# Performance work log

Hardware: AMD Instinct MI355X
Metric: run time of the kernel (lower is better)

## Reference

```python
import jax, jax.numpy as jnp
import numpy as np

BS, SD, SL, HS = 8, 200, 96, 64
GDEP = 2
ALPHA = 0.1
EPS = 1e-5


def _ln(x, g, b):
    # LayerNorm over the last 3 dims (matches nn.LayerNorm([d1,d2,d3]))
    mu = x.mean((-3, -2, -1), keepdims=True)
    var = x.var((-3, -2, -1), keepdims=True)
    return (x - mu) * jax.lax.rsqrt(var + EPS) * g + b


def _gru(x, Wih, Whh, bih, bhh):
    # single-layer batch_first GRU, returns output sequence. x: [B, L, H]
    B, L, H = x.shape
    xw = x @ Wih.T + bih  # precompute input projections [B, L, 3H]

    def step(h, xw_t):
        gh = h @ Whh.T + bhh
        xr, xz, xn = jnp.split(xw_t, 3, -1)
        hr, hz, hn = jnp.split(gh, 3, -1)
        r = jax.nn.sigmoid(xr + hr)
        z = jax.nn.sigmoid(xz + hz)
        n = jnp.tanh(xn + r * hn)
        h = (1.0 - z) * n + z * h
        return h, h

    _, ys = jax.lax.scan(step, jnp.zeros((B, H), x.dtype), jnp.swapaxes(xw, 0, 1))
    return jnp.swapaxes(ys, 0, 1)


def _norm_adj(A):
    # add self loops, row-normalize (MTGNN mixprop preprocessing)
    Ah = A + jnp.eye(A.shape[-1], dtype=A.dtype)
    return Ah / Ah.sum(-1, keepdims=True)


def _mixprop(x, a, W, b):
    # x: [B, C, V, L], a: [V, V] (static graph)
    h = x
    outs = [h]
    for _ in range(GDEP):
        h = ALPHA * x + (1.0 - ALPHA) * jnp.einsum('bcwl,vw->bcvl', h, a)
        outs.append(h)
    ho = jnp.concatenate(outs, axis=1)  # [B, (GDEP+1)C, V, L]
    return jnp.einsum('bcvl,oc->bovl', ho, W) + b[None, :, None, None]


def _dyna_mixprop(x, a, W, b):
    # x: [B, C, V, L], a: [B, L, V, W] (per-batch, per-time dynamic graph)
    h = x
    outs = [h]
    for _ in range(GDEP):
        h = ALPHA * x + (1.0 - ALPHA) * jnp.einsum('bcwl,blvw->bcvl', h, a)
        outs.append(h)
    ho = jnp.concatenate(outs, axis=1)
    return jnp.einsum('bcvl,oc->bovl', ho, W) + b[None, :, None, None]


def _fwd(x, adj, dyna_adj, g1, b1, g2, b2, Wih, Whh, bih, bhh,
         Wg1, bg1, Wg2, bg2, Wd1, bd1, Wd2, bd2, Wm, bm):
    bs, sd, sl, hs = x.shape
    # RNN encoder over time with residual
    xr = _gru(_ln(x, g1, b1).reshape(bs * sd, sl, hs), Wih, Whh, bih, bhh) \
        + x.reshape(bs * sd, sl, hs)
    xc = xr.reshape(bs, sd, sl, hs).transpose(0, 3, 1, 2)  # [bs, hs, sd, sl]
    nx = _ln(xc, g2, b2)
    a = _norm_adj(adj)
    at = _norm_adj(adj.T)
    da = _norm_adj(dyna_adj)
    dat = _norm_adj(jnp.swapaxes(dyna_adj, -1, -2))
    x_static = (_mixprop(nx, a, Wg1, bg1) + _mixprop(nx, at, Wg2, bg2)).transpose(0, 2, 3, 1)
    x_dyna = (_dyna_mixprop(nx, da, Wd1, bd1) + _dyna_mixprop(nx, dat, Wd2, bd2)).transpose(0, 2, 3, 1)
    merged = jnp.concatenate([x_static, x_dyna], axis=-1) @ Wm.T + bm
    return merged + xc.transpose(0, 2, 3, 1)  # [bs, sd, sl, hs]


def setup_inputs() -> dict:
    key = jax.random.key(0)
    ks = jax.random.split(key, 20)
    s = 0.02
    C3 = (GDEP + 1) * HS
    return {
        'x': jax.random.normal(ks[0], (BS, SD, SL, HS), jnp.float32),
        'adj': jax.random.uniform(ks[1], (SD, SD), jnp.float32),
        'dyna_adj': jax.random.uniform(ks[2], (BS, SL, SD, SD), jnp.float32),
        'g1': 1.0 + s * jax.random.normal(ks[3], (SD, SL, HS), jnp.float32),
        'b1': s * jax.random.normal(ks[4], (SD, SL, HS), jnp.float32),
        'g2': 1.0 + s * jax.random.normal(ks[5], (HS, SD, SL), jnp.float32),
        'b2': s * jax.random.normal(ks[6], (HS, SD, SL), jnp.float32),
        'Wih': s * jax.random.normal(ks[7], (3 * HS, HS), jnp.float32),
        'Whh': s * jax.random.normal(ks[8], (3 * HS, HS), jnp.float32),
        'bih': jnp.zeros((3 * HS,), jnp.float32),
        'bhh': jnp.zeros((3 * HS,), jnp.float32),
        'Wg1': s * jax.random.normal(ks[9], (HS, C3), jnp.float32),
        'bg1': jnp.zeros((HS,), jnp.float32),
        'Wg2': s * jax.random.normal(ks[10], (HS, C3), jnp.float32),
        'bg2': jnp.zeros((HS,), jnp.float32),
        'Wd1': s * jax.random.normal(ks[11], (HS, C3), jnp.float32),
        'bd1': jnp.zeros((HS,), jnp.float32),
        'Wd2': s * jax.random.normal(ks[12], (HS, C3), jnp.float32),
        'bd2': jnp.zeros((HS,), jnp.float32),
        'Wm': s * jax.random.normal(ks[13], (HS, 2 * HS), jnp.float32),
        'bm': jnp.zeros((HS,), jnp.float32),
    }


def reference(x, adj, dyna_adj, g1, b1, g2, b2, Wih, Whh, bih, bhh,
              Wg1, bg1, Wg2, bg2, Wd1, bd1, Wd2, bd2, Wm, bm):
    return _fwd(x, adj, dyna_adj, g1, b1, g2, b2, Wih, Whh, bih, bhh,
                Wg1, bg1, Wg2, bg2, Wd1, bd1, Wd2, bd2, Wm, bm)
```

## Files before the change

### kernel.cpp

```cpp
#include <hip/hip_runtime.h>
#include <math.h>

#define ALPHA_ 0.1f
#define BETA_  0.9f
#define EPS_   1e-5f

typedef __bf16 bf16x8 __attribute__((ext_vector_type(8)));
typedef float f32x16 __attribute__((ext_vector_type(16)));

__device__ __forceinline__ unsigned short f2bf(float f) {
    return __builtin_bit_cast(unsigned short, (__bf16)f);
}
__device__ __forceinline__ float bf2f(unsigned short u) {
    return (float)__builtin_bit_cast(__bf16, u);
}

__device__ __forceinline__ float wave_reduce_sum(float v) {
#pragma unroll
    for (int off = 32; off > 0; off >>= 1) v += __shfl_down(v, off, 64);
    return v;
}

__global__ void k_ln_part(const float4* __restrict__ x4, float2* __restrict__ part) {
    const int b = blockIdx.y, jb = blockIdx.x, t = threadIdx.x;
    const size_t base = (size_t)b * 307200 + (size_t)jb * 4096;
    float s = 0.f, sq = 0.f;
#pragma unroll
    for (int k = 0; k < 16; k++) {
        float4 v = x4[base + k * 256 + t];
        s  += v.x + v.y + v.z + v.w;
        sq += v.x * v.x + v.y * v.y + v.z * v.z + v.w * v.w;
    }
    float rs = wave_reduce_sum(s);
    float rq = wave_reduce_sum(sq);
    __shared__ float2 ws[4];
    if ((t & 63) == 0) ws[t >> 6] = make_float2(rs, rq);
    __syncthreads();
    if (t == 0) {
        float a = 0.f, q = 0.f;
        for (int k = 0; k < 4; k++) { a += ws[k].x; q += ws[k].y; }
        part[b * 75 + jb] = make_float2(a, q);
    }
}

__global__ void k_ln_final(const float2* __restrict__ part, int nper, float2* __restrict__ outp) {
    const int b = blockIdx.x, t = threadIdx.x;
    float s = 0.f, sq = 0.f;
    for (int p = t; p < nper; p += 64) {
        float2 v = part[b * nper + p];
        s += v.x; sq += v.y;
    }
    s  = wave_reduce_sum(s);
    sq = wave_reduce_sum(sq);
    if (t == 0) {
        const float invN = 1.f / 1228800.f;
        float mu  = s * invN;
        float var = sq * invN - mu * mu;
        outp[b] = make_float2(mu, rsqrtf(var + EPS_));
    }
}

__global__ __launch_bounds__(256) void k_xw2(const float* __restrict__ x,
        const float* __restrict__ g1, const float* __restrict__ b1,
        const float2* __restrict__ s1, const float* __restrict__ Wih,
        const float* __restrict__ bih, unsigned short* __restrict__ xw) {
    __shared__ unsigned short sXb[128 * 64];
    __shared__ unsigned short sWb[192 * 64];
    const int t = threadIdx.x;
    const int R0 = blockIdx.x * 128;
    const float2 st1 = s1[R0 / 19200];
    for (int idx = t; idx < 8192; idx += 256) {
        int rr = idx >> 6, cc = idx & 63;
        int row = R0 + rr;
        int gi = (row % 19200) * 64 + cc;
        float v = (x[(size_t)row * 64 + cc] - st1.x) * st1.y * g1[gi] + b1[gi];
        *(unsigned short*)((char*)sXb + ((rr * 128 + cc * 2) ^ ((rr & 7) << 4))) = f2bf(v);
    }
    for (int idx = t; idx < 12288; idx += 256) {
        int j = idx >> 6, k = idx & 63;
        *(unsigned short*)((char*)sWb + ((j * 128 + k * 2) ^ ((j & 7) << 4))) = f2bf(Wih[idx]);
    }
    __syncthreads();
    const int wid = t >> 6, lane = t & 63, ln = lane & 31, hl = lane >> 5;
    f32x16 acc[6] = {};
#pragma unroll
    for (int ks = 0; ks < 4; ks++) {
        int ao = ((wid * 32 + ln) * 128 + ks * 32 + hl * 16) ^ ((ln & 7) << 4);
        bf16x8 af = __builtin_bit_cast(bf16x8, *(const uint4*)((const char*)sXb + ao));
#pragma unroll
        for (int nt = 0; nt < 6; nt++) {
            int bo = ((nt * 32 + ln) * 128 + ks * 32 + hl * 16) ^ ((ln & 7) << 4);
            bf16x8 bfr = __builtin_bit_cast(bf16x8, *(const uint4*)((const char*)sWb + bo));
            acc[nt] = __builtin_amdgcn_mfma_f32_32x32x16_bf16(af, bfr, acc[nt], 0, 0, 0);
        }
    }
#pragma unroll
    for (int nt = 0; nt < 6; nt++) {
        float bi = bih[nt * 32 + ln];
#pragma unroll
        for (int reg = 0; reg < 16; reg++) {
            int rrow = (reg & 3) + 8 * (reg >> 2) + 4 * hl;
            int row = R0 + wid * 32 + rrow;
            xw[(size_t)row * 192 + nt * 32 + ln] = f2bf(acc[nt][reg] + bi);
        }
    }
}

__global__ __launch_bounds__(512) void k_gru2(const unsigned short* __restrict__ xw,
        const float* __restrict__ x, const float* __restrict__ Whh,
        const float* __restrict__ bhh, float* __restrict__ xr, float2* __restrict__ s2p) {
    __shared__ unsigned short hb[2048];
    __shared__ float gh[1536];
    __shared__ float2 sRed[8];
    const int t = threadIdx.x;
    const int wid = t >> 6, lane = t & 63, ln = lane & 31, hl = lane >> 5;
    const int row0 = blockIdx.x * 8;
    const int r = wid;
    const int c = t & 63;

    bf16x8 Bf[4];
    if (wid < 6) {
        const int j = wid * 32 + ln;
#pragma unroll
        for (int ks = 0; ks < 4; ks++) {
            const float* wp = Whh + j * 64 + ks * 16 + hl * 8;
            float4 w0 = *(const float4*)wp;
            float4 w1 = *(const float4*)(wp + 4);
            bf16x8 bb;
            bb[0] = (__bf16)w0.x; bb[1] = (__bf16)w0.y; bb[2] = (__bf16)w0.z; bb[3] = (__bf16)w0.w;
            bb[4] = (__bf16)w1.x; bb[5] = (__bf16)w1.y; bb[6] = (__bf16)w1.z; bb[7] = (__bf16)w1.w;
            Bf[ks] = bb;
        }
    }
    for (int i = t; i < 2048; i += 512) hb[i] = 0;

    const float b_r = bhh[c], b_z = bhh[64 + c], b_n = bhh[128 + c];
    const unsigned short* xwp = xw + (size_t)(row0 + r) * 96 * 192;
    const float* xp  = x  + (size_t)(row0 + r) * 96 * 64;
    float*       xrp = xr + (size_t)(row0 + r) * 96 * 64;
    float xg = bf2f(xwp[c]), zg = bf2f(xwp[64 + c]), ng = bf2f(xwp[128 + c]);
    float xv = xp[c];
    float h = 0.f, lsum = 0.f, lsq = 0.f;
    __syncthreads();

    for (int st = 0; st < 96; st++) {
        if (wid < 6) {
            f32x16 acc = {};
#pragma unroll
            for (int ks = 0; ks < 4; ks++) {
                int ao = (ln * 128 + ks * 32 + hl * 16) ^ ((ln & 7) << 4);
                bf16x8 af = __builtin_bit_cast(bf16x8, *(const uint4*)((const char*)hb + ao));
                acc = __builtin_amdgcn_mfma_f32_32x32x16_bf16(af, Bf[ks], acc, 0, 0, 0);
            }
#pragma unroll
            for (int reg = 0; reg < 4; reg++) {
                gh[(reg + 4 * hl) * 192 + wid * 32 + ln] = acc[reg];
            }
        }
        __syncthreads();
        float hr_ = gh[r * 192 + c] + b_r;
        float hz  = gh[r * 192 + 64 + c] + b_z;
        float hn  = gh[r * 192 + 128 + c] + b_n;
        float rg_ = 1.f / (1.f + __expf(-(xg + hr_)));
        float zg_ = 1.f / (1.f + __expf(-(zg + hz)));
        float ny = ng + rg_ * hn;
        ny = fminf(fmaxf(ny, -15.f), 15.f);
        float e2 = __expf(-2.f * ny);
        float nv = (1.f - e2) / (1.f + e2);
        h = nv + zg_ * (h - nv);
        float ov = h + xv;
        xrp[st * 64 + c] = ov;
        lsum += ov; lsq += ov * ov;
        *(unsigned short*)((char*)hb + ((r * 128 + c * 2) ^ ((r & 7) << 4))) = f2bf(h);
        int sn = st < 95 ? st + 1 : 95;
        xg = bf2f(xwp[sn * 192 + c]); zg = bf2f(xwp[sn * 192 + 64 + c]); ng = bf2f(xwp[sn * 192 + 128 + c]);
        xv = xp[sn * 64 + c];
        __syncthreads();
    }
    float s = wave_reduce_sum(lsum);
    float q = wave_reduce_sum(lsq);
    if (lane == 0) sRed[wid] = make_float2(s, q);
    __syncthreads();
    if (t == 0) {
        float a = 0.f, b_ = 0.f;
        for (int k = 0; k < 8; k++) { a += sRed[k].x; b_ += sRed[k].y; }
        s2p[blockIdx.x] = make_float2(a, b_);
    }
}

__global__ void k_tr(const float* __restrict__ in, float* __restrict__ outp) {
    __shared__ float tile[32][33];
    const int v = blockIdx.x;
    const int ct = blockIdx.y & 1;
    const int lt = blockIdx.y >> 1;
    const int t = threadIdx.x;
    const int lx = t & 31, ly = t >> 5;
    const int c0 = ct * 32, l0 = lt * 32;
#pragma unroll
    for (int q = 0; q < 4; q++) {
        int cc = ly + q * 8;
        tile[cc][lx] = in[(size_t)(c0 + cc) * 19200 + (size_t)v * 96 + l0 + lx];
    }
    __syncthreads();
#pragma unroll
    for (int q = 0; q < 4; q++) {
        int ll = ly + q * 8;
        outp[(size_t)(l0 + ll) * 12800 + (size_t)v * 64 + c0 + lx] = tile[lx][ll];
    }
}

__global__ void k_adjprep2(const float* __restrict__ adj, unsigned short* __restrict__ an_b,
        unsigned short* __restrict__ atn_b) {
    const int v = blockIdx.x;
    const int mode = blockIdx.y;
    const int t = threadIdx.x;
    unsigned short* outp = (mode == 0) ? an_b : atn_b;
    float val = 0.f;
    if (t < 200) val = (mode == 0) ? adj[v * 200 + t] : adj[t * 200 + v];
    float s = wave_reduce_sum(val);
    __shared__ float sp[4];
    if ((t & 63) == 0) sp[t >> 6] = s;
    __syncthreads();
    float inv = 1.f / (sp[0] + sp[1] + sp[2] + sp[3] + 1.f);
    if (t < 208) {
        float o = (t < 200) ? (val + (t == v ? 1.f : 0.f)) * inv : 0.f;
        outp[(((t >> 3) * 200) + v) * 8 + (t & 7)] = f2bf(o);
    }
}

__global__ __launch_bounds__(512) void k_dprep4(const float* __restrict__ dyna,
        unsigned short* __restrict__ danr, unsigned short* __restrict__ danc) {
    __shared__ unsigned short sT[200 * 201];
    __shared__ float sRow[200];
    __shared__ float sColP[8][256];
    __shared__ float sInv[416];
    const int blk = blockIdx.x;
    const int t = threadIdx.x;
    const int lane = t & 63, rq = t >> 6;
    const float* S = dyna + (size_t)blk * 40000;
    float colacc[4] = {0.f, 0.f, 0.f, 0.f};
    for (int p = 0; p < 25; p++) {
        const int r = p * 8 + rq;
        float rsum = 0.f;
#pragma unroll
        for (int s = 0; s < 4; s++) {
            const int c = s * 64 + lane;
            if (c < 200) {
                float v = S[r * 200 + c] + ((r == c) ? 1.f : 0.f);
                sT[c * 201 + r] = f2bf(v);
                rsum += v;
                colacc[s] += v;
            }
        }
        float rs = wave_reduce_sum(rsum);
        if (lane == 0) sRow[r] = rs;
    }
#pragma unroll
    for (int s = 0; s < 4; s++) sColP[rq][s * 64 + lane] = colacc[s];
    __syncthreads();
    if (t < 200) {
        sInv[t] = 1.f / sRow[t];
        float cs = 0.f;
#pragma unroll
        for (int q = 0; q < 8; q++) cs += sColP[q][t];
        sInv[208 + t] = 1.f / cs;
    }
    __syncthreads();
    unsigned short* dr = danr + (size_t)blk * 41600;
    unsigned short* dc = danc + (size_t)blk * 41600;
    for (int item = t; item < 5200; item += 512) {
        const int cch = item / 200;
        const int v = item - cch * 200;
        const float irv = sInv[v];
        const float icv = sInv[208 + v];
        unsigned short rb[8], cb[8];
#pragma unroll
        for (int j = 0; j < 8; j++) {
            const int w = cch * 8 + j;
            float fr = 0.f, fc = 0.f;
            if (w < 200) {
                fr = bf2f(sT[w * 201 + v]) * irv;
                fc = bf2f(sT[v * 201 + w]) * icv;
            }
            rb[j] = f2bf(fr); cb[j] = f2bf(fc);
        }
        *(uint4*)&dr[item * 8] = make_uint4(
            (unsigned)rb[0] | ((unsigned)rb[1] << 16), (unsigned)rb[2] | ((unsigned)rb[3] << 16),
            (unsigned)rb[4] | ((unsigned)rb[5] << 16), (unsigned)rb[6] | ((unsigned)rb[7] << 16));
        *(uint4*)&dc[item * 8] = make_uint4(
            (unsigned)cb[0] | ((unsigned)cb[1] << 16), (unsigned)cb[2] | ((unsigned)cb[3] << 16),
            (unsigned)cb[4] | ((unsigned)cb[5] << 16), (unsigned)cb[6] | ((unsigned)cb[7] << 16));
    }
}

__global__ void k_meff(const float* __restrict__ Wm, const float* __restrict__ Wg1,
        const float* __restrict__ Wg2, const float* __restrict__ Wd1, const float* __restrict__ Wd2,
        const float* __restrict__ bg1, const float* __restrict__ bg2, const float* __restrict__ bd1,
        const float* __restrict__ bd2, const float* __restrict__ bm,
        float* __restrict__ MeffF, float* __restrict__ biasE) {
    const int k = blockIdx.x;
    const int t = threadIdx.x;
    const int o = t >> 2;
    const int cb = (t & 3) * 16;
    float acc[16];
#pragma unroll
    for (int q = 0; q < 16; q++) acc[q] = 0.f;
    if (k == 0) {
        for (int m = 0; m < 64; m++) {
            float aL = Wm[o * 128 + m], aR = Wm[o * 128 + 64 + m];
#pragma unroll
            for (int q = 0; q < 16; q++) {
                int cc = cb + q;
                acc[q] += aL * (Wg1[m * 192 + cc] + Wg2[m * 192 + cc])
                        + aR * (Wd1[m * 192 + cc] + Wd2[m * 192 + cc]);
            }
        }
    } else {
        const float* Ws = (k <= 2) ? Wg1 : (k <= 4) ? Wg2 : (k <= 6) ? Wd1 : Wd2;
        const int side = (k <= 4) ? 0 : 64;
        const int hop = (((k - 1) & 1) == 0) ? 64 : 128;
        for (int m = 0; m < 64; m++) {
            float a_ = Wm[o * 128 + side + m];
#pragma unroll
            for (int q = 0; q < 16; q++) acc[q] += a_ * Ws[m * 192 + hop + cb + q];
        }
    }
#pragma unroll
    for (int q = 0; q < 16; q++) MeffF[k * 4096 + o * 64 + cb + q] = acc[q];
    if (k == 0 && t < 64) {
        float s = bm[t];
        for (int cc = 0; cc < 64; cc++)
            s += Wm[t * 128 + cc] * (bg1[cc] + bg2[cc]) + Wm[t * 128 + 64 + cc] * (bd1[cc] + bd2[cc]);
        biasE[t] = s;
    }
}

__global__ void k_meffc(const float* __restrict__ MeffF, unsigned short* __restrict__ MeffB) {
    const int t = threadIdx.x;
#pragma unroll 4
    for (int j = 0; j < 16; j++) {
        int idx = t * 16 + j;
        float m[9];
#pragma unroll
        for (int k = 0; k < 9; k++) m[k] = MeffF[k * 4096 + idx];
        float sum = 0.f;
#pragma unroll
        for (int k = 1; k < 9; k++) sum += m[k];
        MeffB[idx] = f2bf(m[0] + ALPHA_ * sum);
#pragma unroll
        for (int c = 0; c < 4; c++) {
            MeffB[(1 + 2 * c) * 4096 + idx] = f2bf(BETA_ * m[1 + 2 * c] + ALPHA_ * BETA_ * m[2 + 2 * c]);
            MeffB[(2 + 2 * c) * 4096 + idx] = f2bf(BETA_ * BETA_ * m[2 + 2 * c]);
        }
    }
}

__global__ void k_nx(const float4* __restrict__ xr4, const float2* __restrict__ s2,
        const float4* __restrict__ g2t4, const float4* __restrict__ b2t4,
        unsigned short* __restrict__ nxb) {
    size_t id = (size_t)blockIdx.x * 256 + threadIdx.x;
    int cf = (int)(id & 15);
    size_t grp = id >> 4;
    int v = (int)(grp % 200);
    size_t bl = grp / 200;
    int l = (int)(bl % 96);
    int b = (int)(bl / 96);
    float2 st = s2[b];
    float4 xv = xr4[(((size_t)(b * 200 + v)) * 96 + l) * 16 + cf];
    size_t gi = ((size_t)l * 200 + v) * 16 + cf;
    float4 g = g2t4[gi];
    float4 bb = b2t4[gi];
    unsigned int lo = (unsigned)f2bf((xv.x - st.x) * st.y * g.x + bb.x)
                    | ((unsigned)f2bf((xv.y - st.x) * st.y * g.y + bb.y) << 16);
    unsigned int hi = (unsigned)f2bf((xv.z - st.x) * st.y * g.z + bb.z)
                    | ((unsigned)f2bf((xv.w - st.x) * st.y * g.w + bb.w) << 16);
    ((uint2*)nxb)[id] = make_uint2(lo, hi);
}

#define OFF_A 0
#define OFF_HTA 83968
#define OFF_HTB 110592
#define OFF_OBUF 0
#define SMEM10 137216

__device__ __forceinline__ int ht4(int o, int w) {
    return (o * 416 + w * 2) ^ ((o & 7) << 4);
}

__device__ __forceinline__ void store_tile_bf16(unsigned char* smem, int off, const f32x16& val,
        int mt, int ocol, int half) {
#pragma unroll
    for (int g = 0; g < 4; g++) {
        const int wv = mt * 32 + half * 4 + g * 8;
        if (wv < 200) {
            unsigned short pk[4];
#pragma unroll
            for (int i = 0; i < 4; i++) pk[i] = f2bf(val[g * 4 + i]);
            *(uint2*)(smem + off + ht4(ocol, wv)) = make_uint2(
                (unsigned)pk[0] | ((unsigned)pk[1] << 16),
                (unsigned)pk[2] | ((unsigned)pk[3] << 16));
        }
    }
}

__device__ __forceinline__ void stageA(const unsigned short* __restrict__ A,
        unsigned char* smem, int t) {
#pragma unroll
    for (int i = 0; i < 5; i++) {
        const int idx = t + i * 1024;
        __builtin_amdgcn_global_load_lds(
            (const __attribute__((address_space(1))) unsigned int*)(const void*)(A + (size_t)idx * 8),
            (__attribute__((address_space(3))) unsigned int*)(void*)(smem + OFF_A + idx * 16),
            16, 0, 0);
    }
    if (t < 80) {
        const int idx = 5120 + t;
        *(uint4*)(smem + OFF_A + idx * 16) = *(const uint4*)(const void*)(A + (size_t)idx * 8);
    }
}

__global__ __launch_bounds__(1024) void k_graph10(const unsigned short* __restrict__ nxb,
        const float* __restrict__ xrb, const unsigned short* __restrict__ an_b,
        const unsigned short* __restrict__ atn_b, const unsigned short* __restrict__ danr_b,
        const unsigned short* __restrict__ danc_b, const unsigned short* __restrict__ MeffB,
        const float* __restrict__ biasE, float* __restrict__ out) {
    __shared__ __align__(16) unsigned char smem[SMEM10];
    const int blk = blockIdx.x;
    const int b = blk / 96, l = blk % 96;
    const int t = threadIdx.x;
    const int wid = t >> 6, lane = t & 63, ln = lane & 31, half = lane >> 5;
    const bool act = (wid < 14);
    const int mt = wid >> 1, ot = wid & 1;
    const int ocol = ot * 32 + ln;
    const int vr = mt * 32 + ln;
    const int ar = (vr < 200) ? vr : 0;
    const bool vz = (vr >= 200);

    const unsigned short* Achain[4] = { an_b, atn_b,
        danr_b + (size_t)blk * 41600, danc_b + (size_t)blk * 41600 };

    uint4 h0f[4] = {};
    if (act && !vz) {
        const unsigned short* H0p = nxb + (size_t)blk * 12800 + vr * 64;
#pragma unroll
        for (int kk = 0; kk < 4; kk++) {
            h0f[kk] = *(const uint4*)(const void*)(H0p + kk * 16 + half * 8);
        }
    }

    stageA(Achain[0], smem, t);
    if (t < 512) {
        int o = t >> 3, w = 200 + (t & 7);
        *(unsigned short*)(smem + OFF_HTA + ht4(o, w)) = 0;
        *(unsigned short*)(smem + OFF_HTB + ht4(o, w)) = 0;
    }
    __syncthreads();

    f32x16 ACC = {};
    if (act) {
        const unsigned short* MBf = MeffB;
        const unsigned short* MB2 = MeffB + 2 * 4096;
        f32x16 y2 = {};
#pragma unroll
        for (int kk = 0; kk < 4; kk++) {
            const int c0 = kk * 16 + half * 8;
            bf16x8 h0 = __builtin_bit_cast(bf16x8, h0f[kk]);
            bf16x8 mf = __builtin_bit_cast(bf16x8, *(const uint4*)(const void*)(MBf + ocol * 64 + c0));
            ACC = __builtin_amdgcn_mfma_f32_32x32x16_bf16(h0, mf, ACC, 0, 0, 0);
            bf16x8 m2 = __builtin_bit_cast(bf16x8, *(const uint4*)(const void*)(MB2 + ocol * 64 + c0));
            y2 = __builtin_amdgcn_mfma_f32_32x32x16_bf16(h0, m2, y2, 0, 0, 0);
        }
        store_tile_bf16(smem, OFF_HTA, y2, mt, ocol, half);
    }
    __syncthreads();

#pragma unroll 1
    for (int chain = 0; chain < 4; chain++) {
        if (act) {
            const unsigned short* MB1 = MeffB + (size_t)(1 + 2 * chain) * 4096;
            f32x16 T = {};
#pragma unroll
            for (int kk = 0; kk < 4; kk++) {
                const int c0 = kk * 16 + half * 8;
                bf16x8 h0 = __builtin_bit_cast(bf16x8, h0f[kk]);
                bf16x8 m1 = __builtin_bit_cast(bf16x8, *(const uint4*)(const void*)(MB1 + ocol * 64 + c0));
                T = __builtin_amdgcn_mfma_f32_32x32x16_bf16(h0, m1, T, 0, 0, 0);
            }
#pragma unroll
            for (int kk = 0; kk < 13; kk++) {
                const int k0 = kk * 16 + half * 8;
                uint4 av = *(const uint4*)(smem + OFF_A + (((2 * kk + half) * 200 + ar) << 4));
                if (vz) av = make_uint4(0, 0, 0, 0);
                bf16x8 yb = __builtin_bit_cast(bf16x8, *(const uint4*)(smem + OFF_HTA + ht4(ocol, k0)));
                T = __builtin_amdgcn_mfma_f32_32x32x16_bf16(
                    __builtin_bit_cast(bf16x8, av), yb, T, 0, 0, 0);
            }
            store_tile_bf16(smem, OFF_HTB, T, mt, ocol, half);
        }
        __syncthreads();
        if (act) {
#pragma unroll
            for (int kk = 0; kk < 13; kk++) {
                const int k0 = kk * 16 + half * 8;
                uint4 av = *(const uint4*)(smem + OFF_A + (((2 * kk + half) * 200 + ar) << 4));
                if (vz) av = make_uint4(0, 0, 0, 0);
                bf16x8 ub = __builtin_bit_cast(bf16x8, *(const uint4*)(smem + OFF_HTB + ht4(ocol, k0)));
                ACC = __builtin_amdgcn_mfma_f32_32x32x16_bf16(
                    __builtin_bit_cast(bf16x8, av), ub, ACC, 0, 0, 0);
            }
        }
        __syncthreads();
        if (chain < 3) {
            stageA(Achain[chain + 1], smem, t);
            if (act) {
                const unsigned short* MB2n = MeffB + (size_t)(4 + 2 * chain) * 4096;
                f32x16 y2 = {};
#pragma unroll
                for (int kk = 0; kk < 4; kk++) {
                    const int c0 = kk * 16 + half * 8;
                    bf16x8 h0 = __builtin_bit_cast(bf16x8, h0f[kk]);
                    bf16x8 m2 = __builtin_bit_cast(bf16x8, *(const uint4*)(const void*)(MB2n + ocol * 64 + c0));
                    y2 = __builtin_amdgcn_mfma_f32_32x32x16_bf16(h0, m2, y2, 0, 0, 0);
                }
                store_tile_bf16(smem, OFF_HTA, y2, mt, ocol, half);
            }
            __syncthreads();
        }
    }

    __syncthreads();
    if (act) {
#pragma unroll
        for (int r = 0; r < 16; r++) {
            const int v = mt * 32 + half * 4 + (r & 3) + (r >> 2) * 8;
            if (v < 200) *(float*)(smem + OFF_OBUF + (v * 64 + ocol) * 4) = ACC[r];
        }
    }
    __syncthreads();

    const size_t gbase = ((size_t)b * 200 * 96 + l) * 64;
    for (int idx = t; idx < 12800; idx += 1024) {
        int v = idx >> 6, o = idx & 63;
        float val = *(const float*)(smem + OFF_OBUF + idx * 4) + biasE[o];
        size_t gi = gbase + (size_t)v * 6144 + o;
        out[gi] = val + xrb[gi];
    }
}

extern "C" void kernel_launch(void* const* d_in, const int* in_sizes, int n_in,
                              void* d_out, int out_size, void* d_ws, size_t ws_size,
                              hipStream_t stream) {
    (void)in_sizes; (void)n_in; (void)out_size; (void)ws_size;
    const float* x    = (const float*)d_in[0];
    const float* adj  = (const float*)d_in[1];
    const float* dyna = (const float*)d_in[2];
    const float* g1   = (const float*)d_in[3];
    const float* b1   = (const float*)d_in[4];
    const float* g2   = (const float*)d_in[5];
    const float* b2   = (const float*)d_in[6];
    const float* Wih  = (const float*)d_in[7];
    const float* Whh  = (const float*)d_in[8];
    const float* bih  = (const float*)d_in[9];
    const float* bhh  = (const float*)d_in[10];
    const float* Wg1  = (const float*)d_in[11];
    const float* bg1  = (const float*)d_in[12];
    const float* Wg2  = (const float*)d_in[13];
    const float* bg2  = (const float*)d_in[14];
    const float* Wd1  = (const float*)d_in[15];
    const float* bd1  = (const float*)d_in[16];
    const float* Wd2  = (const float*)d_in[17];
    const float* bd2  = (const float*)d_in[18];
    const float* Wm   = (const float*)d_in[19];
    const float* bm   = (const float*)d_in[20];
    float* out = (float*)d_out;
    float* ws = (float*)d_ws;

    float*          xr    = ws;
    unsigned short* nxb   = (unsigned short*)(ws + 9830400);
    float*          g2t   = ws + 14745600;
    float*          b2t   = ws + 15974400;
    unsigned short* an_b  = (unsigned short*)(ws + 17203200);
    unsigned short* atn_b = (unsigned short*)(ws + 17226496);
    unsigned short* MeffB = (unsigned short*)(ws + 17249792);
    float*          biasE = ws + 17268224;
    float2*         s1p   = (float2*)(ws + 17268288);
    float2*         s1    = (float2*)(ws + 17269488);
    float2*         s2p   = (float2*)(ws + 17269504);
    float2*         s2    = (float2*)(ws + 17269904);
    float*          MeffF = ws + 17269920;
    unsigned short* xwb    = (unsigned short*)(ws + 17306784);
    unsigned short* danr_b = (unsigned short*)(ws + 17306784);
    unsigned short* danc_b = danr_b + 31953792;

    k_ln_part<<<dim3(75, 8), dim3(256), 0, stream>>>((const float4*)x, s1p);
    k_ln_final<<<dim3(8), dim3(64), 0, stream>>>(s1p, 75, s1);
    k_xw2<<<dim3(1200), dim3(256), 0, stream>>>(x, g1, b1, s1, Wih, bih, xwb);
    k_gru2<<<dim3(200), dim3(512), 0, stream>>>(xwb, x, Whh, bhh, xr, s2p);
    k_ln_final<<<dim3(8), dim3(64), 0, stream>>>(s2p, 25, s2);
    k_tr<<<dim3(200, 6), dim3(256), 0, stream>>>(g2, g2t);
    k_tr<<<dim3(200, 6), dim3(256), 0, stream>>>(b2, b2t);
    k_adjprep2<<<dim3(200, 2), dim3(256), 0, stream>>>(adj, an_b, atn_b);
    k_meff<<<dim3(9), dim3(256), 0, stream>>>(Wm, Wg1, Wg2, Wd1, Wd2, bg1, bg2, bd1, bd2, bm, MeffF, biasE);
    k_meffc<<<dim3(1), dim3(256), 0, stream>>>(MeffF, MeffB);
    k_nx<<<dim3(9600), dim3(256), 0, stream>>>((const float4*)xr, s2, (const float4*)g2t, (const float4*)b2t, nxb);
    k_dprep4<<<dim3(768), dim3(512), 0, stream>>>(dyna, danr_b, danc_b);
    k_graph10<<<dim3(768), dim3(1024), 0, stream>>>(nxb, xr, an_b, atn_b, danr_b, danc_b, MeffB, biasE, out);
}
```

Before: 436.5 us.

## Fuse GRU input projection into recurrent kernel and widen dyna-adj prep blocks

Drops the separate input-projection GEMM kernel. The recurrent GRU kernel now applies the first LayerNorm on the fly and computes x·Wih together with h·Whh in one MFMA chain of K=128, with separate n-gate accumulators so r·hn stays correct. This removes the bf16 xw intermediate write and read, but puts extra MFMA work and global loads of x/g1/b1 on the serial 96-step critical path. The dynamic-adjacency prep kernel also moves from 512 to 1024 threads per block to spread the row loop across more waves.

```diff
diff --git a/kernel.cpp b/kernel.cpp
--- a/kernel.cpp
+++ b/kernel.cpp
@@ -60,70 +60,33 @@
     }
 }
 
-__global__ __launch_bounds__(256) void k_xw2(const float* __restrict__ x,
+__global__ __launch_bounds__(512) void k_gru3(const float* __restrict__ x,
         const float* __restrict__ g1, const float* __restrict__ b1,
         const float2* __restrict__ s1, const float* __restrict__ Wih,
-        const float* __restrict__ bih, unsigned short* __restrict__ xw) {
-    __shared__ unsigned short sXb[128 * 64];
-    __shared__ unsigned short sWb[192 * 64];
-    const int t = threadIdx.x;
-    const int R0 = blockIdx.x * 128;
-    const float2 st1 = s1[R0 / 19200];
-    for (int idx = t; idx < 8192; idx += 256) {
-        int rr = idx >> 6, cc = idx & 63;
-        int row = R0 + rr;
-        int gi = (row % 19200) * 64 + cc;
-        float v = (x[(size_t)row * 64 + cc] - st1.x) * st1.y * g1[gi] + b1[gi];
-        *(unsigned short*)((char*)sXb + ((rr * 128 + cc * 2) ^ ((rr & 7) << 4))) = f2bf(v);
-    }
-    for (int idx = t; idx < 12288; idx += 256) {
-        int j = idx >> 6, k = idx & 63;
-        *(unsigned short*)((char*)sWb + ((j * 128 + k * 2) ^ ((j & 7) << 4))) = f2bf(Wih[idx]);
-    }
-    __syncthreads();
-    const int wid = t >> 6, lane = t & 63, ln = lane & 31, hl = lane >> 5;
-    f32x16 acc[6] = {};
-#pragma unroll
-    for (int ks = 0; ks < 4; ks++) {
-        int ao = ((wid * 32 + ln) * 128 + ks * 32 + hl * 16) ^ ((ln & 7) << 4);
-        bf16x8 af = __builtin_bit_cast(bf16x8, *(const uint4*)((const char*)sXb + ao));
-#pragma unroll
-        for (int nt = 0; nt < 6; nt++) {
-            int bo = ((nt * 32 + ln) * 128 + ks * 32 + hl * 16) ^ ((ln & 7) << 4);
-            bf16x8 bfr = __builtin_bit_cast(bf16x8, *(const uint4*)((const char*)sWb + bo));
-            acc[nt] = __builtin_amdgcn_mfma_f32_32x32x16_bf16(af, bfr, acc[nt], 0, 0, 0);
-        }
-    }
-#pragma unroll
-    for (int nt = 0; nt < 6; nt++) {
-        float bi = bih[nt * 32 + ln];
-#pragma unroll
-        for (int reg = 0; reg < 16; reg++) {
-            int rrow = (reg & 3) + 8 * (reg >> 2) + 4 * hl;
-            int row = R0 + wid * 32 + rrow;
-            xw[(size_t)row * 192 + nt * 32 + ln] = f2bf(acc[nt][reg] + bi);
-        }
-    }
-}
-
-__global__ __launch_bounds__(512) void k_gru2(const unsigned short* __restrict__ xw,
-        const float* __restrict__ x, const float* __restrict__ Whh,
+        const float* __restrict__ Whh, const float* __restrict__ bih,
         const float* __restrict__ bhh, float* __restrict__ xr, float2* __restrict__ s2p) {
-    __shared__ unsigned short hb[2048];
-    __shared__ float gh[1536];
+    __shared__ unsigned short hb[32 * 128];
+    __shared__ float gh[8 * 192];
+    __shared__ float ghn[8 * 64];
     __shared__ float2 sRed[8];
     const int t = threadIdx.x;
     const int wid = t >> 6, lane = t & 63, ln = lane & 31, hl = lane >> 5;
     const int row0 = blockIdx.x * 8;
     const int r = wid;
     const int c = t & 63;
-
-    bf16x8 Bf[4];
+    const int row = row0 + r;
+    const int sd = row % 200;
+    const int bidx = row / 200;
+    const bool isN = (wid >= 4 && wid < 6);
+
+    bf16x8 Bf[8];
     if (wid < 6) {
         const int j = wid * 32 + ln;
 #pragma unroll
-        for (int ks = 0; ks < 4; ks++) {
-            const float* wp = Whh + j * 64 + ks * 16 + hl * 8;
+        for (int ks = 0; ks < 8; ks++) {
+            const float* Wsrc = (ks < 4) ? Wih : Whh;
+            const int kk = (ks & 3) * 16 + hl * 8;
+            const float* wp = Wsrc + j * 64 + kk;
             float4 w0 = *(const float4*)wp;
             float4 w1 = *(const float4*)(wp + 4);
             bf16x8 bb;
@@ -132,38 +95,66 @@
             Bf[ks] = bb;
         }
     }
-    for (int i = t; i < 2048; i += 512) hb[i] = 0;
-
-    const float b_r = bhh[c], b_z = bhh[64 + c], b_n = bhh[128 + c];
-    const unsigned short* xwp = xw + (size_t)(row0 + r) * 96 * 192;
-    const float* xp  = x  + (size_t)(row0 + r) * 96 * 64;
-    float*       xrp = xr + (size_t)(row0 + r) * 96 * 64;
-    float xg = bf2f(xwp[c]), zg = bf2f(xwp[64 + c]), ng = bf2f(xwp[128 + c]);
+    for (int i = t; i < 4096; i += 512) hb[i] = 0;
+    __syncthreads();
+
+    const float b_r = bih[c] + bhh[c];
+    const float b_z = bih[64 + c] + bhh[64 + c];
+    const float bx_n = bih[128 + c];
+    const float bh_n = bhh[128 + c];
+    const float2 st1 = s1[bidx];
+    const float* xp  = x  + (size_t)row * 96 * 64;
+    const float* gp  = g1 + (size_t)sd * 96 * 64;
+    const float* bp  = b1 + (size_t)sd * 96 * 64;
+    float*       xrp = xr + (size_t)row * 96 * 64;
+
     float xv = xp[c];
+    {
+        float xln = (xv - st1.x) * st1.y * gp[c] + bp[c];
+        *(unsigned short*)((char*)hb + ((r * 256 + c * 2) ^ ((r & 7) << 4))) = f2bf(xln);
+    }
     float h = 0.f, lsum = 0.f, lsq = 0.f;
     __syncthreads();
 
     for (int st = 0; st < 96; st++) {
-        if (wid < 6) {
+        if (wid < 4) {
             f32x16 acc = {};
 #pragma unroll
-            for (int ks = 0; ks < 4; ks++) {
-                int ao = (ln * 128 + ks * 32 + hl * 16) ^ ((ln & 7) << 4);
+            for (int ks = 0; ks < 8; ks++) {
+                int ao = (ln * 256 + ks * 32 + hl * 16) ^ ((ln & 7) << 4);
                 bf16x8 af = __builtin_bit_cast(bf16x8, *(const uint4*)((const char*)hb + ao));
                 acc = __builtin_amdgcn_mfma_f32_32x32x16_bf16(af, Bf[ks], acc, 0, 0, 0);
             }
 #pragma unroll
+            for (int reg = 0; reg < 4; reg++)
+                gh[(reg + 4 * hl) * 192 + wid * 32 + ln] = acc[reg];
+        } else if (isN) {
+            f32x16 accx = {}, acch = {};
+#pragma unroll
+            for (int ks = 0; ks < 4; ks++) {
+                int aox = (ln * 256 + ks * 32 + hl * 16) ^ ((ln & 7) << 4);
+                bf16x8 afx = __builtin_bit_cast(bf16x8, *(const uint4*)((const char*)hb + aox));
+                accx = __builtin_amdgcn_mfma_f32_32x32x16_bf16(afx, Bf[ks], accx, 0, 0, 0);
+                int aoh = (ln * 256 + (ks + 4) * 32 + hl * 16) ^ ((ln & 7) << 4);
+                bf16x8 afh = __builtin_bit_cast(bf16x8, *(const uint4*)((const char*)hb + aoh));
+                acch = __builtin_amdgcn_mfma_f32_32x32x16_bf16(afh, Bf[ks + 4], acch, 0, 0, 0);
+            }
+#pragma unroll
             for (int reg = 0; reg < 4; reg++) {
-                gh[(reg + 4 * hl) * 192 + wid * 32 + ln] = acc[reg];
-            }
-        }
+                gh[(reg + 4 * hl) * 192 + wid * 32 + ln] = accx[reg];
+                ghn[(reg + 4 * hl) * 64 + (wid - 4) * 32 + ln] = acch[reg];
+            }
+        }
+        int sn = st < 95 ? st + 1 : 95;
+        float xv_n = xp[sn * 64 + c];
+        float g1_n = gp[sn * 64 + c];
+        float b1_n = bp[sn * 64 + c];
         __syncthreads();
-        float hr_ = gh[r * 192 + c] + b_r;
-        float hz  = gh[r * 192 + 64 + c] + b_z;
-        float hn  = gh[r * 192 + 128 + c] + b_n;
-        float rg_ = 1.f / (1.f + __expf(-(xg + hr_)));
-        float zg_ = 1.f / (1.f + __expf(-(zg + hz)));
-        float ny = ng + rg_ * hn;
+        float rg_ = 1.f / (1.f + __expf(-(gh[r * 192 + c] + b_r)));
+        float zg_ = 1.f / (1.f + __expf(-(gh[r * 192 + 64 + c] + b_z)));
+        float xn = gh[r * 192 + 128 + c] + bx_n;
+        float hn = ghn[r * 64 + c] + bh_n;
+        float ny = xn + rg_ * hn;
         ny = fminf(fmaxf(ny, -15.f), 15.f);
         float e2 = __expf(-2.f * ny);
         float nv = (1.f - e2) / (1.f + e2);
@@ -171,10 +162,10 @@
         float ov = h + xv;
         xrp[st * 64 + c] = ov;
         lsum += ov; lsq += ov * ov;
-        *(unsigned short*)((char*)hb + ((r * 128 + c * 2) ^ ((r & 7) << 4))) = f2bf(h);
-        int sn = st < 95 ? st + 1 : 95;
-        xg = bf2f(xwp[sn * 192 + c]); zg = bf2f(xwp[sn * 192 + 64 + c]); ng = bf2f(xwp[sn * 192 + 128 + c]);
-        xv = xp[sn * 64 + c];
+        *(unsigned short*)((char*)hb + ((r * 256 + (64 + c) * 2) ^ ((r & 7) << 4))) = f2bf(h);
+        float xln = (xv_n - st1.x) * st1.y * g1_n + b1_n;
+        *(unsigned short*)((char*)hb + ((r * 256 + c * 2) ^ ((r & 7) << 4))) = f2bf(xln);
+        xv = xv_n;
         __syncthreads();
     }
     float s = wave_reduce_sum(lsum);
@@ -228,32 +219,34 @@
     }
 }
 
-__global__ __launch_bounds__(512) void k_dprep4(const float* __restrict__ dyna,
+__global__ __launch_bounds__(1024) void k_dprep5(const float* __restrict__ dyna,
         unsigned short* __restrict__ danr, unsigned short* __restrict__ danc) {
     __shared__ unsigned short sT[200 * 201];
     __shared__ float sRow[200];
-    __shared__ float sColP[8][256];
+    __shared__ float sColP[16][256];
     __shared__ float sInv[416];
     const int blk = blockIdx.x;
     const int t = threadIdx.x;
     const int lane = t & 63, rq = t >> 6;
     const float* S = dyna + (size_t)blk * 40000;
     float colacc[4] = {0.f, 0.f, 0.f, 0.f};
-    for (int p = 0; p < 25; p++) {
-        const int r = p * 8 + rq;
-        float rsum = 0.f;
-#pragma unroll
-        for (int s = 0; s < 4; s++) {
-            const int c = s * 64 + lane;
-            if (c < 200) {
-                float v = S[r * 200 + c] + ((r == c) ? 1.f : 0.f);
-                sT[c * 201 + r] = f2bf(v);
-                rsum += v;
-                colacc[s] += v;
-            }
-        }
-        float rs = wave_reduce_sum(rsum);
-        if (lane == 0) sRow[r] = rs;
+    for (int p = 0; p < 13; p++) {
+        const int r = p * 16 + rq;
+        if (r < 200) {
+            float rsum = 0.f;
+#pragma unroll
+            for (int s = 0; s < 4; s++) {
+                const int c = s * 64 + lane;
+                if (c < 200) {
+                    float v = S[r * 200 + c] + ((r == c) ? 1.f : 0.f);
+                    sT[c * 201 + r] = f2bf(v);
+                    rsum += v;
+                    colacc[s] += v;
+                }
+            }
+            float rs = wave_reduce_sum(rsum);
+            if (lane == 0) sRow[r] = rs;
+        }
     }
 #pragma unroll
     for (int s = 0; s < 4; s++) sColP[rq][s * 64 + lane] = colacc[s];
@@ -262,13 +255,13 @@
         sInv[t] = 1.f / sRow[t];
         float cs = 0.f;
 #pragma unroll
-        for (int q = 0; q < 8; q++) cs += sColP[q][t];
+        for (int q = 0; q < 16; q++) cs += sColP[q][t];
         sInv[208 + t] = 1.f / cs;
     }
     __syncthreads();
     unsigned short* dr = danr + (size_t)blk * 41600;
     unsigned short* dc = danc + (size_t)blk * 41600;
-    for (int item = t; item < 5200; item += 512) {
+    for (int item = t; item < 5200; item += 1024) {
         const int cch = item / 200;
         const int v = item - cch * 200;
         const float irv = sInv[v];
@@ -588,14 +581,12 @@
     float2*         s2p   = (float2*)(ws + 17269504);
     float2*         s2    = (float2*)(ws + 17269904);
     float*          MeffF = ws + 17269920;
-    unsigned short* xwb    = (unsigned short*)(ws + 17306784);
     unsigned short* danr_b = (unsigned short*)(ws + 17306784);
     unsigned short* danc_b = danr_b + 31953792;
 
     k_ln_part<<<dim3(75, 8), dim3(256), 0, stream>>>((const float4*)x, s1p);
     k_ln_final<<<dim3(8), dim3(64), 0, stream>>>(s1p, 75, s1);
-    k_xw2<<<dim3(1200), dim3(256), 0, stream>>>(x, g1, b1, s1, Wih, bih, xwb);
-    k_gru2<<<dim3(200), dim3(512), 0, stream>>>(xwb, x, Whh, bhh, xr, s2p);
+    k_gru3<<<dim3(200), dim3(512), 0, stream>>>(x, g1, b1, s1, Wih, Whh, bih, bhh, xr, s2p);
     k_ln_final<<<dim3(8), dim3(64), 0, stream>>>(s2p, 25, s2);
     k_tr<<<dim3(200, 6), dim3(256), 0, stream>>>(g2, g2t);
     k_tr<<<dim3(200, 6), dim3(256), 0, stream>>>(b2, b2t);
@@ -603,6 +594,6 @@
     k_meff<<<dim3(9), dim3(256), 0, stream>>>(Wm, Wg1, Wg2, Wd1, Wd2, bg1, bg2, bd1, bd2, bm, MeffF, biasE);
     k_meffc<<<dim3(1), dim3(256), 0, stream>>>(MeffF, MeffB);
     k_nx<<<dim3(9600), dim3(256), 0, stream>>>((const float4*)xr, s2, (const float4*)g2t, (const float4*)b2t, nxb);
-    k_dprep4<<<dim3(768), dim3(512), 0, stream>>>(dyna, danr_b, danc_b);
+    k_dprep5<<<dim3(768), dim3(1024), 0, stream>>>(dyna, danr_b, danc_b);
     k_graph10<<<dim3(768), dim3(1024), 0, stream>>>(nxb, xr, an_b, atn_b, danr_b, danc_b, MeffB, biasE, out);
 }
```

Result: faster. 405.1 us (median of 2 runs) (-7.2%).
